# Kernel optimization log

Measured on AMD Instinct MI355X. Metric: run time of the kernel, lower is better.

The kernel has to match this reference:

```python
import jax, jax.numpy as jnp
import numpy as np

B, IN, H = 16384, 512, 512


def setup_inputs() -> dict:
    key = jax.random.key(0)
    ks = jax.random.split(key, 7)
    s_in = 1.0 / np.sqrt(IN)
    s_h = 1.0 / np.sqrt(H)
    return {
        "x": jax.random.normal(ks[0], (B, IN), jnp.float32),
        "h": jax.random.normal(ks[1], (B, H), jnp.float32),
        "c": jax.random.normal(ks[2], (B, H), jnp.float32),
        # packed gate weights, order [i, f, g, o] along last dim (4*H)
        "Wx": jax.random.normal(ks[3], (IN, 4 * H), jnp.float32) * s_in,
        "Wh": jax.random.normal(ks[4], (H, 4 * H), jnp.float32) * s_h,
        "bx": jax.random.normal(ks[5], (4 * H,), jnp.float32) * s_in,
        "bh": jax.random.normal(ks[6], (4 * H,), jnp.float32) * s_h,
    }


def reference(x, h, c, Wx, Wh, bx, bh):
    # one fused GEMM per input stream instead of 8 small linears; same math
    gates = x @ Wx + bx + h @ Wh + bh          # [B, 4H]
    gi, gf, gg, go = jnp.split(gates, 4, axis=-1)
    i = jax.nn.sigmoid(gi)
    f = jax.nn.sigmoid(gf)
    g = jnp.tanh(gg)
    o = jax.nn.sigmoid(go)
    c_new = f * c + i * g
    h_new = o * jnp.tanh(c_new)
    return (h_new, c_new)
```

## Files before the change

### kernel.cpp

```cpp
#include <hip/hip_runtime.h>
#include <hip/hip_bf16.h>

#define B_DIM   16384
#define IN_DIM  512
#define H_DIM   512
#define K_DIM   1024
#define N4H     2048
#define BH      (B_DIM * H_DIM)

typedef __attribute__((ext_vector_type(8))) short  short8;
typedef __attribute__((ext_vector_type(4))) short  short4v;
typedef __attribute__((ext_vector_type(4))) float  f32x4;

__device__ inline void async_load16(const void* g, void* l) {
    __builtin_amdgcn_global_load_lds(
        (const __attribute__((address_space(1))) void*)g,
        (__attribute__((address_space(3)))       void*)l, 16, 0, 0);
}

__device__ inline short bf16bits(float f) {
    __hip_bfloat16 b = __float2bfloat16(f);
    return *reinterpret_cast<short*>(&b);
}

__device__ inline float sigmoidf_(float v) {
    return 1.0f / (1.0f + __expf(-v));
}
__device__ inline float tanhf_(float v) {
    v = fminf(fmaxf(v, -30.f), 30.f);
    float e = __expf(2.f * v);
    return (e - 1.f) / (e + 1.f);
}

__global__ __launch_bounds__(256) void prep_all(
    const float* __restrict__ Wx, const float* __restrict__ Wh,
    const float* __restrict__ bx, const float* __restrict__ bh,
    const float* __restrict__ x,  const float* __restrict__ h,
    __hip_bfloat16* __restrict__ Wt, __hip_bfloat16* __restrict__ Axh,
    float* __restrict__ bias_p) {
    const int bid = blockIdx.x;
    const int t   = threadIdx.x;

    if (bid < 2048) {
        __shared__ __hip_bfloat16 tile[32][33];
        const int bk = bid & 31;
        const int bn = bid >> 5;
        const int kb = bk * 32, nb = bn * 32;
#pragma unroll
        for (int r = 0; r < 4; ++r) {
            int k_loc = r * 8 + (t >> 5);
            int n_loc = t & 31;
            int kg = kb + k_loc;
            float v = (kg < IN_DIM) ? Wx[(size_t)kg * N4H + nb + n_loc]
                                    : Wh[(size_t)(kg - IN_DIM) * N4H + nb + n_loc];
            tile[k_loc][n_loc] = __float2bfloat16(v);
        }
        __syncthreads();
        {
            int n_loc = t >> 3;
            int k_loc = (t & 7) * 4;
            int ng = nb + n_loc;
            int g  = ng >> 9;
            int c  = ng & 511;
            int row_out = (c >> 5) * 128 + g * 32 + (c & 31);
            short4v v4;
            v4.x = *reinterpret_cast<short*>(&tile[k_loc + 0][n_loc]);
            v4.y = *reinterpret_cast<short*>(&tile[k_loc + 1][n_loc]);
            v4.z = *reinterpret_cast<short*>(&tile[k_loc + 2][n_loc]);
            v4.w = *reinterpret_cast<short*>(&tile[k_loc + 3][n_loc]);
            *(short4v*)&Wt[(size_t)row_out * K_DIM + kb + k_loc] = v4;
        }
        if (bid < 8) {
            int ng = bid * 256 + t;
            int g  = ng >> 9;
            int c  = ng & 511;
            int ro = (c >> 5) * 128 + g * 32 + (c & 31);
            bias_p[ro] = bx[ng] + bh[ng];
        }
    } else {
        const int ab = bid - 2048;
        const int kq = t;
        const float* src = (kq < 128) ? (x + kq * 4)
                                      : (h + (size_t)(kq - 128) * 4);
#pragma unroll
        for (int j = 0; j < 8; ++j) {
            int m = ab * 8 + j;
            float4 v = *(const float4*)(src + (size_t)m * 512);
            short4v sv;
            sv.x = bf16bits(v.x);
            sv.y = bf16bits(v.y);
            sv.z = bf16bits(v.z);
            sv.w = bf16bits(v.w);
            *(short4v*)&Axh[(size_t)m * K_DIM + kq * 4] = sv;
        }
    }
}

__global__ __launch_bounds__(256, 3) void lstm_gemm(
    const float* __restrict__ c_in,
    const __hip_bfloat16* __restrict__ Axh,
    const __hip_bfloat16* __restrict__ Wt,
    const float* __restrict__ bias_p,
    float* __restrict__ out) {
    __shared__ __hip_bfloat16 lds_a[128 * 32];
    __shared__ __hip_bfloat16 lds_b[128 * 32];

    const int tid   = threadIdx.x;
    const int w     = tid >> 6;
    const int lane  = tid & 63;
    const int col16 = lane & 15;
    const int quad  = lane >> 4;

    const int jb    = blockIdx.x;
    const int xcd   = jb & 7;
    const int local = jb >> 3;
    const int bm    = xcd * 16 + (local >> 4);
    const int bn    = local & 15;

    f32x4 acc[2][8];
#pragma unroll
    for (int mi = 0; mi < 2; ++mi)
#pragma unroll
        for (int ni = 0; ni < 8; ++ni)
            acc[mi][ni] = (f32x4){0.f, 0.f, 0.f, 0.f};

    const __hip_bfloat16* Ab = Axh + (size_t)bm * 128 * K_DIM;
    const __hip_bfloat16* Bb = Wt  + (size_t)bn * 128 * K_DIM;

    const int s0 = w * 128 + lane;
    const int s1 = s0 + 64;
    const int r0 = s0 >> 2, r1 = s1 >> 2;
    const int q0 = ((s0 & 3) - ((r0 >> 1) & 3)) & 3;
    const int q1 = ((s1 & 3) - ((r1 >> 1) & 3)) & 3;
    const size_t ga0 = (size_t)r0 * K_DIM + q0 * 8;
    const size_t ga1 = (size_t)r1 * K_DIM + q1 * 8;
    __hip_bfloat16* la0 = lds_a + w * 1024;
    __hip_bfloat16* la1 = lds_a + w * 1024 + 512;
    __hip_bfloat16* lb0 = lds_b + w * 1024;
    __hip_bfloat16* lb1 = lds_b + w * 1024 + 512;

    int aoff[2], boff[8];
#pragma unroll
    for (int mi = 0; mi < 2; ++mi) {
        int r = w * 32 + mi * 16 + col16;
        aoff[mi] = (r * 4 + ((quad + ((r >> 1) & 3)) & 3)) * 16;
    }
#pragma unroll
    for (int ni = 0; ni < 8; ++ni) {
        int r = ni * 16 + col16;
        boff[ni] = (r * 4 + ((quad + ((r >> 1) & 3)) & 3)) * 16;
    }
    const char* lap = (const char*)lds_a;
    const char* lbp = (const char*)lds_b;

    for (int kt = 0; kt < 32; ++kt) {
        const int kb = kt * 32;
        async_load16(Ab + ga0 + kb, la0);
        async_load16(Ab + ga1 + kb, la1);
        async_load16(Bb + ga0 + kb, lb0);
        async_load16(Bb + ga1 + kb, lb1);
        __syncthreads();

        short8 afr[2], bfr[8];
#pragma unroll
        for (int mi = 0; mi < 2; ++mi)
            afr[mi] = *(const short8*)(lap + aoff[mi]);
#pragma unroll
        for (int ni = 0; ni < 8; ++ni)
            bfr[ni] = *(const short8*)(lbp + boff[ni]);
#pragma unroll
        for (int mi = 0; mi < 2; ++mi)
#pragma unroll
            for (int ni = 0; ni < 8; ++ni)
                acc[mi][ni] = __builtin_amdgcn_mfma_f32_16x16x32_bf16(
                    afr[mi], bfr[ni], acc[mi][ni], 0, 0, 0);
        __syncthreads();
    }

    float bias_v[4][2];
#pragma unroll
    for (int g = 0; g < 4; ++g)
#pragma unroll
        for (int h2 = 0; h2 < 2; ++h2)
            bias_v[g][h2] = bias_p[bn * 128 + g * 32 + h2 * 16 + col16];

#pragma unroll
    for (int mi = 0; mi < 2; ++mi) {
#pragma unroll
        for (int reg = 0; reg < 4; ++reg) {
            const int m_g = bm * 128 + w * 32 + mi * 16 + quad * 4 + reg;
#pragma unroll
            for (int h2 = 0; h2 < 2; ++h2) {
                const int hc_g = bn * 32 + h2 * 16 + col16;
                float gi = acc[mi][0 + h2][reg] + bias_v[0][h2];
                float gf = acc[mi][2 + h2][reg] + bias_v[1][h2];
                float gg = acc[mi][4 + h2][reg] + bias_v[2][h2];
                float go = acc[mi][6 + h2][reg] + bias_v[3][h2];
                float iv = sigmoidf_(gi);
                float fv = sigmoidf_(gf);
                float gv = tanhf_(gg);
                float ov = sigmoidf_(go);
                float co = c_in[(size_t)m_g * H_DIM + hc_g];
                float cn = fv * co + iv * gv;
                float hn = ov * tanhf_(cn);
                out[(size_t)m_g * H_DIM + hc_g]      = hn;
                out[BH + (size_t)m_g * H_DIM + hc_g] = cn;
            }
        }
    }
}

__global__ __launch_bounds__(256) void prep_weights_fb(
    const float* __restrict__ Wx, const float* __restrict__ Wh,
    const float* __restrict__ bx, const float* __restrict__ bh,
    __hip_bfloat16* __restrict__ Wt, float* __restrict__ bias_p) {
    __shared__ __hip_bfloat16 tile[32][33];
    const int bid = blockIdx.x;
    const int bk  = bid & 31;
    const int bn  = bid >> 5;
    const int t   = threadIdx.x;
    const int kb  = bk * 32, nb = bn * 32;
#pragma unroll
    for (int r = 0; r < 4; ++r) {
        int k_loc = r * 8 + (t >> 5);
        int n_loc = t & 31;
        int kg = kb + k_loc;
        float v = (kg < IN_DIM) ? Wx[(size_t)kg * N4H + nb + n_loc]
                                : Wh[(size_t)(kg - IN_DIM) * N4H + nb + n_loc];
        tile[k_loc][n_loc] = __float2bfloat16(v);
    }
    __syncthreads();
    {
        int n_loc = t >> 3;
        int k_loc = (t & 7) * 4;
        int ng = nb + n_loc;
        int g  = ng >> 9;
        int c  = ng & 511;
        int row_out = (c >> 5) * 128 + g * 32 + (c & 31);
        short4v v4;
        v4.x = *reinterpret_cast<short*>(&tile[k_loc + 0][n_loc]);
        v4.y = *reinterpret_cast<short*>(&tile[k_loc + 1][n_loc]);
        v4.z = *reinterpret_cast<short*>(&tile[k_loc + 2][n_loc]);
        v4.w = *reinterpret_cast<short*>(&tile[k_loc + 3][n_loc]);
        *(short4v*)&Wt[(size_t)row_out * K_DIM + kb + k_loc] = v4;
    }
    if (bid < 8) {
        int ng = bid * 256 + t;
        int g  = ng >> 9;
        int c  = ng & 511;
        int ro = (c >> 5) * 128 + g * 32 + (c & 31);
        bias_p[ro] = bx[ng] + bh[ng];
    }
}

__global__ __launch_bounds__(256, 3) void lstm_gemm_fb(
    const float* __restrict__ x, const float* __restrict__ h,
    const float* __restrict__ c_in,
    const __hip_bfloat16* __restrict__ Wt, const float* __restrict__ bias_p,
    float* __restrict__ out) {
    __shared__ __hip_bfloat16 lds_a[128 * 32];
    __shared__ __hip_bfloat16 lds_b[128 * 32];
    const int tid   = threadIdx.x;
    const int bn    = blockIdx.x & 15;
    const int bm    = blockIdx.x >> 4;
    const int w     = tid >> 6;
    const int lane  = tid & 63;
    const int col16 = lane & 15;
    const int quad  = lane >> 4;
    f32x4 acc[2][8];
#pragma unroll
    for (int mi = 0; mi < 2; ++mi)
#pragma unroll
        for (int ni = 0; ni < 8; ++ni)
            acc[mi][ni] = (f32x4){0.f, 0.f, 0.f, 0.f};
    const __hip_bfloat16* wt_base = Wt + (size_t)(bn * 128) * K_DIM;
    const int chunk0 = w * 2;
    const int e0     = chunk0 * 512 + lane * 8;
    const int bn_loc0 = e0 >> 5, bk_off0 = e0 & 31;
    const int e1     = (chunk0 + 1) * 512 + lane * 8;
    const int bn_loc1 = e1 >> 5, bk_off1 = e1 & 31;
    for (int kt = 0; kt < 32; ++kt) {
        const int kb = kt * 32;
        const float* aptr;
        int koff;
        if (kb < IN_DIM) { aptr = x; koff = kb; }
        else             { aptr = h; koff = kb - IN_DIM; }
        async_load16(wt_base + (size_t)bn_loc0 * K_DIM + kb + bk_off0,
                     (void*)(lds_b + chunk0 * 512));
        async_load16(wt_base + (size_t)bn_loc1 * K_DIM + kb + bk_off1,
                     (void*)(lds_b + (chunk0 + 1) * 512));
        float4 av[4];
#pragma unroll
        for (int j = 0; j < 4; ++j) {
            int cch = j * 256 + tid;
            int row = cch >> 3;
            int kq  = (cch & 7) * 4;
            av[j] = *(const float4*)(aptr + (size_t)(bm * 128 + row) * IN_DIM
                                     + koff + kq);
        }
#pragma unroll
        for (int j = 0; j < 4; ++j) {
            int cch = j * 256 + tid;
            int row = cch >> 3;
            int kq  = (cch & 7) * 4;
            short4v sv;
            sv.x = bf16bits(av[j].x);
            sv.y = bf16bits(av[j].y);
            sv.z = bf16bits(av[j].z);
            sv.w = bf16bits(av[j].w);
            *(short4v*)&lds_a[row * 32 + kq] = sv;
        }
        __syncthreads();
        short8 afr[2], bfr[8];
#pragma unroll
        for (int mi = 0; mi < 2; ++mi)
            afr[mi] = *(const short8*)&lds_a[(w * 32 + mi * 16 + col16) * 32 + quad * 8];
#pragma unroll
        for (int ni = 0; ni < 8; ++ni)
            bfr[ni] = *(const short8*)&lds_b[(ni * 16 + col16) * 32 + quad * 8];
#pragma unroll
        for (int mi = 0; mi < 2; ++mi)
#pragma unroll
            for (int ni = 0; ni < 8; ++ni)
                acc[mi][ni] = __builtin_amdgcn_mfma_f32_16x16x32_bf16(
                    afr[mi], bfr[ni], acc[mi][ni], 0, 0, 0);
        __syncthreads();
    }
    float bias_v[4][2];
#pragma unroll
    for (int g = 0; g < 4; ++g)
#pragma unroll
        for (int h2 = 0; h2 < 2; ++h2)
            bias_v[g][h2] = bias_p[bn * 128 + g * 32 + h2 * 16 + col16];
#pragma unroll
    for (int mi = 0; mi < 2; ++mi) {
#pragma unroll
        for (int reg = 0; reg < 4; ++reg) {
            const int m_g = bm * 128 + w * 32 + mi * 16 + quad * 4 + reg;
#pragma unroll
            for (int h2 = 0; h2 < 2; ++h2) {
                const int hc_g = bn * 32 + h2 * 16 + col16;
                float gi = acc[mi][0 + h2][reg] + bias_v[0][h2];
                float gf = acc[mi][2 + h2][reg] + bias_v[1][h2];
                float gg = acc[mi][4 + h2][reg] + bias_v[2][h2];
                float go = acc[mi][6 + h2][reg] + bias_v[3][h2];
                float iv = sigmoidf_(gi);
                float fv = sigmoidf_(gf);
                float gv = tanhf_(gg);
                float ov = sigmoidf_(go);
                float co = c_in[(size_t)m_g * H_DIM + hc_g];
                float cn = fv * co + iv * gv;
                float hn = ov * tanhf_(cn);
                out[(size_t)m_g * H_DIM + hc_g]      = hn;
                out[BH + (size_t)m_g * H_DIM + hc_g] = cn;
            }
        }
    }
}

extern "C" void kernel_launch(void* const* d_in, const int* in_sizes, int n_in,
                              void* d_out, int out_size, void* d_ws, size_t ws_size,
                              hipStream_t stream) {
    const float* x  = (const float*)d_in[0];
    const float* h  = (const float*)d_in[1];
    const float* c  = (const float*)d_in[2];
    const float* Wx = (const float*)d_in[3];
    const float* Wh = (const float*)d_in[4];
    const float* bx = (const float*)d_in[5];
    const float* bh = (const float*)d_in[6];

    const size_t wtBytes  = (size_t)N4H * K_DIM * 2;
    const size_t axhBytes = (size_t)B_DIM * K_DIM * 2;
    const size_t need     = wtBytes + axhBytes + (size_t)N4H * 4;

    if (ws_size >= need) {
        __hip_bfloat16* Wt  = (__hip_bfloat16*)d_ws;
        __hip_bfloat16* Axh = (__hip_bfloat16*)((char*)d_ws + wtBytes);
        float* bias_p = (float*)((char*)d_ws + wtBytes + axhBytes);
        prep_all<<<4096, 256, 0, stream>>>(Wx, Wh, bx, bh, x, h, Wt, Axh, bias_p);
        lstm_gemm<<<2048, 256, 0, stream>>>(c, Axh, Wt, bias_p, (float*)d_out);
    } else {
        __hip_bfloat16* Wt = (__hip_bfloat16*)d_ws;
        float* bias_p = (float*)((char*)d_ws + wtBytes);
        prep_weights_fb<<<2048, 256, 0, stream>>>(Wx, Wh, bx, bh, Wt, bias_p);
        lstm_gemm_fb<<<2048, 256, 0, stream>>>(x, h, c, Wt, bias_p, (float*)d_out);
    }
}
```

Baseline: 250.8 us.

## Switch LSTM GEMM to 32x32x16 MFMA with BK=64 and XOR-swizzled LDS

Replaces the 16x16x32 bf16 MFMA tiling with 32x32x16 MFMA, so each wave computes a 32x128 tile with four accumulators. The K step per iteration doubles to 64, which halves the number of barrier pairs, and the LDS layout moves to an XOR swizzle to avoid bank conflicts. The c_in values are now prefetched into registers before the main loop so their latency overlaps the GEMM. The occupancy hint rises to 4 blocks per CU, which risks register spills with 64 accumulator floats plus 16 prefetched c values per thread.

```diff
diff --git a/kernel.cpp b/kernel.cpp
--- a/kernel.cpp
+++ b/kernel.cpp
@@ -8,9 +8,10 @@
 #define N4H     2048
 #define BH      (B_DIM * H_DIM)
 
-typedef __attribute__((ext_vector_type(8))) short  short8;
-typedef __attribute__((ext_vector_type(4))) short  short4v;
-typedef __attribute__((ext_vector_type(4))) float  f32x4;
+typedef __attribute__((ext_vector_type(8)))  short  short8;
+typedef __attribute__((ext_vector_type(4)))  short  short4v;
+typedef __attribute__((ext_vector_type(4)))  float  f32x4;
+typedef __attribute__((ext_vector_type(16))) float  f32x16;
 
 __device__ inline void async_load16(const void* g, void* l) {
     __builtin_amdgcn_global_load_lds(
@@ -96,20 +97,20 @@
     }
 }
 
-__global__ __launch_bounds__(256, 3) void lstm_gemm(
+__global__ __launch_bounds__(256, 4) void lstm_gemm(
     const float* __restrict__ c_in,
     const __hip_bfloat16* __restrict__ Axh,
     const __hip_bfloat16* __restrict__ Wt,
     const float* __restrict__ bias_p,
     float* __restrict__ out) {
-    __shared__ __hip_bfloat16 lds_a[128 * 32];
-    __shared__ __hip_bfloat16 lds_b[128 * 32];
-
-    const int tid   = threadIdx.x;
-    const int w     = tid >> 6;
-    const int lane  = tid & 63;
-    const int col16 = lane & 15;
-    const int quad  = lane >> 4;
+    __shared__ __hip_bfloat16 lds_a[128 * 64];
+    __shared__ __hip_bfloat16 lds_b[128 * 64];
+
+    const int tid  = threadIdx.x;
+    const int w    = tid >> 6;
+    const int lane = tid & 63;
+    const int l31  = lane & 31;
+    const int half = lane >> 5;
 
     const int jb    = blockIdx.x;
     const int xcd   = jb & 7;
@@ -117,96 +118,89 @@
     const int bm    = xcd * 16 + (local >> 4);
     const int bn    = local & 15;
 
-    f32x4 acc[2][8];
-#pragma unroll
-    for (int mi = 0; mi < 2; ++mi)
-#pragma unroll
-        for (int ni = 0; ni < 8; ++ni)
-            acc[mi][ni] = (f32x4){0.f, 0.f, 0.f, 0.f};
+    f32x16 acc[4];
+#pragma unroll
+    for (int ni = 0; ni < 4; ++ni)
+#pragma unroll
+        for (int r = 0; r < 16; ++r)
+            acc[ni][r] = 0.f;
 
     const __hip_bfloat16* Ab = Axh + (size_t)bm * 128 * K_DIM;
     const __hip_bfloat16* Bb = Wt  + (size_t)bn * 128 * K_DIM;
 
-    const int s0 = w * 128 + lane;
-    const int s1 = s0 + 64;
-    const int r0 = s0 >> 2, r1 = s1 >> 2;
-    const int q0 = ((s0 & 3) - ((r0 >> 1) & 3)) & 3;
-    const int q1 = ((s1 & 3) - ((r1 >> 1) & 3)) & 3;
-    const size_t ga0 = (size_t)r0 * K_DIM + q0 * 8;
-    const size_t ga1 = (size_t)r1 * K_DIM + q1 * 8;
-    __hip_bfloat16* la0 = lds_a + w * 1024;
-    __hip_bfloat16* la1 = lds_a + w * 1024 + 512;
-    __hip_bfloat16* lb0 = lds_b + w * 1024;
-    __hip_bfloat16* lb1 = lds_b + w * 1024 + 512;
-
-    int aoff[2], boff[8];
-#pragma unroll
-    for (int mi = 0; mi < 2; ++mi) {
-        int r = w * 32 + mi * 16 + col16;
-        aoff[mi] = (r * 4 + ((quad + ((r >> 1) & 3)) & 3)) * 16;
-    }
-#pragma unroll
-    for (int ni = 0; ni < 8; ++ni) {
-        int r = ni * 16 + col16;
-        boff[ni] = (r * 4 + ((quad + ((r >> 1) & 3)) & 3)) * 16;
-    }
-    const char* lap = (const char*)lds_a;
+    const int r_base = w * 32 + (lane >> 3);
+    const int q8     = (((lane & 7) ^ ((lane >> 3) & 7)) * 8);
+    size_t g_off[4];
+    __hip_bfloat16* lA[4];
+    __hip_bfloat16* lB[4];
+#pragma unroll
+    for (int j = 0; j < 4; ++j) {
+        g_off[j] = (size_t)(r_base + j * 8) * K_DIM + q8;
+        lA[j] = lds_a + w * 2048 + j * 512;
+        lB[j] = lds_b + w * 2048 + j * 512;
+    }
+
+    int rd_off[4];
+#pragma unroll
+    for (int sk = 0; sk < 4; ++sk)
+        rd_off[sk] = l31 * 128 + (((sk * 2 + half) ^ (lane & 7)) * 16);
+
+    const int col = bn * 32 + l31;
+    float c_reg[16];
+#pragma unroll
+    for (int reg = 0; reg < 16; ++reg) {
+        int m_loc = (reg & 3) + 8 * (reg >> 2) + 4 * half;
+        c_reg[reg] = c_in[(size_t)(bm * 128 + w * 32 + m_loc) * H_DIM + col];
+    }
+
+    const char* lap = (const char*)lds_a + w * 4096;
     const char* lbp = (const char*)lds_b;
 
-    for (int kt = 0; kt < 32; ++kt) {
-        const int kb = kt * 32;
-        async_load16(Ab + ga0 + kb, la0);
-        async_load16(Ab + ga1 + kb, la1);
-        async_load16(Bb + ga0 + kb, lb0);
-        async_load16(Bb + ga1 + kb, lb1);
-        __syncthreads();
-
-        short8 afr[2], bfr[8];
-#pragma unroll
-        for (int mi = 0; mi < 2; ++mi)
-            afr[mi] = *(const short8*)(lap + aoff[mi]);
-#pragma unroll
-        for (int ni = 0; ni < 8; ++ni)
-            bfr[ni] = *(const short8*)(lbp + boff[ni]);
-#pragma unroll
-        for (int mi = 0; mi < 2; ++mi)
-#pragma unroll
-            for (int ni = 0; ni < 8; ++ni)
-                acc[mi][ni] = __builtin_amdgcn_mfma_f32_16x16x32_bf16(
-                    afr[mi], bfr[ni], acc[mi][ni], 0, 0, 0);
-        __syncthreads();
-    }
-
-    float bias_v[4][2];
+    for (int kt = 0; kt < 16; ++kt) {
+        const int kb = kt * 64;
+#pragma unroll
+        for (int j = 0; j < 4; ++j) {
+            async_load16(Ab + g_off[j] + kb, lA[j]);
+            async_load16(Bb + g_off[j] + kb, lB[j]);
+        }
+        __syncthreads();
+
+#pragma unroll
+        for (int sk = 0; sk < 4; ++sk) {
+            short8 af = *(const short8*)(lap + rd_off[sk]);
+            short8 bf0 = *(const short8*)(lbp + 0 * 4096 + rd_off[sk]);
+            short8 bf1 = *(const short8*)(lbp + 1 * 4096 + rd_off[sk]);
+            short8 bf2 = *(const short8*)(lbp + 2 * 4096 + rd_off[sk]);
+            short8 bf3 = *(const short8*)(lbp + 3 * 4096 + rd_off[sk]);
+            acc[0] = __builtin_amdgcn_mfma_f32_32x32x16_bf16(af, bf0, acc[0], 0, 0, 0);
+            acc[1] = __builtin_amdgcn_mfma_f32_32x32x16_bf16(af, bf1, acc[1], 0, 0, 0);
+            acc[2] = __builtin_amdgcn_mfma_f32_32x32x16_bf16(af, bf2, acc[2], 0, 0, 0);
+            acc[3] = __builtin_amdgcn_mfma_f32_32x32x16_bf16(af, bf3, acc[3], 0, 0, 0);
+        }
+        __syncthreads();
+    }
+
+    float bias_v[4];
 #pragma unroll
     for (int g = 0; g < 4; ++g)
-#pragma unroll
-        for (int h2 = 0; h2 < 2; ++h2)
-            bias_v[g][h2] = bias_p[bn * 128 + g * 32 + h2 * 16 + col16];
-
-#pragma unroll
-    for (int mi = 0; mi < 2; ++mi) {
-#pragma unroll
-        for (int reg = 0; reg < 4; ++reg) {
-            const int m_g = bm * 128 + w * 32 + mi * 16 + quad * 4 + reg;
-#pragma unroll
-            for (int h2 = 0; h2 < 2; ++h2) {
-                const int hc_g = bn * 32 + h2 * 16 + col16;
-                float gi = acc[mi][0 + h2][reg] + bias_v[0][h2];
-                float gf = acc[mi][2 + h2][reg] + bias_v[1][h2];
-                float gg = acc[mi][4 + h2][reg] + bias_v[2][h2];
-                float go = acc[mi][6 + h2][reg] + bias_v[3][h2];
-                float iv = sigmoidf_(gi);
-                float fv = sigmoidf_(gf);
-                float gv = tanhf_(gg);
-                float ov = sigmoidf_(go);
-                float co = c_in[(size_t)m_g * H_DIM + hc_g];
-                float cn = fv * co + iv * gv;
-                float hn = ov * tanhf_(cn);
-                out[(size_t)m_g * H_DIM + hc_g]      = hn;
-                out[BH + (size_t)m_g * H_DIM + hc_g] = cn;
-            }
-        }
+        bias_v[g] = bias_p[bn * 128 + g * 32 + l31];
+
+#pragma unroll
+    for (int reg = 0; reg < 16; ++reg) {
+        int m_loc = (reg & 3) + 8 * (reg >> 2) + 4 * half;
+        size_t m_g = (size_t)(bm * 128 + w * 32 + m_loc);
+        float gi = acc[0][reg] + bias_v[0];
+        float gf = acc[1][reg] + bias_v[1];
+        float gg = acc[2][reg] + bias_v[2];
+        float go = acc[3][reg] + bias_v[3];
+        float iv = sigmoidf_(gi);
+        float fv = sigmoidf_(gf);
+        float gv = tanhf_(gg);
+        float ov = sigmoidf_(go);
+        float cn = fv * c_reg[reg] + iv * gv;
+        float hn = ov * tanhf_(cn);
+        out[m_g * H_DIM + col]      = hn;
+        out[BH + m_g * H_DIM + col] = cn;
     }
 }
 
```

Result: slower. 281.6 us (+12.3%).

## Double-buffer LDS tiles to prefetch next K-slice during MFMA compute

Applied to the files above, without the earlier changes.

Doubles the shared-memory tiles for A and B. The loop now issues the async global-to-LDS loads for the next K tile right after the barrier, while MFMAs run on the current buffer. This cuts the barriers per iteration from two to one, and is meant to hide global load latency behind compute. The cost is LDS per block going from 16 KB to 32 KB. There is also a risk that the compiler inserts conservative vmcnt waits before the LDS reads, which would cancel the overlap.

```diff
diff --git a/kernel.cpp b/kernel.cpp
--- a/kernel.cpp
+++ b/kernel.cpp
@@ -102,8 +102,8 @@
     const __hip_bfloat16* __restrict__ Wt,
     const float* __restrict__ bias_p,
     float* __restrict__ out) {
-    __shared__ __hip_bfloat16 lds_a[128 * 32];
-    __shared__ __hip_bfloat16 lds_b[128 * 32];
+    __shared__ __hip_bfloat16 lds_a[2][128 * 32];
+    __shared__ __hip_bfloat16 lds_b[2][128 * 32];
 
     const int tid   = threadIdx.x;
     const int w     = tid >> 6;
@@ -134,10 +134,6 @@
     const int q1 = ((s1 & 3) - ((r1 >> 1) & 3)) & 3;
     const size_t ga0 = (size_t)r0 * K_DIM + q0 * 8;
     const size_t ga1 = (size_t)r1 * K_DIM + q1 * 8;
-    __hip_bfloat16* la0 = lds_a + w * 1024;
-    __hip_bfloat16* la1 = lds_a + w * 1024 + 512;
-    __hip_bfloat16* lb0 = lds_b + w * 1024;
-    __hip_bfloat16* lb1 = lds_b + w * 1024 + 512;
 
     int aoff[2], boff[8];
 #pragma unroll
@@ -150,16 +146,24 @@
         int r = ni * 16 + col16;
         boff[ni] = (r * 4 + ((quad + ((r >> 1) & 3)) & 3)) * 16;
     }
-    const char* lap = (const char*)lds_a;
-    const char* lbp = (const char*)lds_b;
+
+    async_load16(Ab + ga0, (void*)(&lds_a[0][w * 1024]));
+    async_load16(Ab + ga1, (void*)(&lds_a[0][w * 1024 + 512]));
+    async_load16(Bb + ga0, (void*)(&lds_b[0][w * 1024]));
+    async_load16(Bb + ga1, (void*)(&lds_b[0][w * 1024 + 512]));
 
     for (int kt = 0; kt < 32; ++kt) {
-        const int kb = kt * 32;
-        async_load16(Ab + ga0 + kb, la0);
-        async_load16(Ab + ga1 + kb, la1);
-        async_load16(Bb + ga0 + kb, lb0);
-        async_load16(Bb + ga1 + kb, lb1);
         __syncthreads();
+        const int p = kt & 1;
+        if (kt < 31) {
+            const int kb = (kt + 1) * 32;
+            async_load16(Ab + ga0 + kb, (void*)(&lds_a[1 - p][w * 1024]));
+            async_load16(Ab + ga1 + kb, (void*)(&lds_a[1 - p][w * 1024 + 512]));
+            async_load16(Bb + ga0 + kb, (void*)(&lds_b[1 - p][w * 1024]));
+            async_load16(Bb + ga1 + kb, (void*)(&lds_b[1 - p][w * 1024 + 512]));
+        }
+        const char* lap = (const char*)lds_a[p];
+        const char* lbp = (const char*)lds_b[p];
 
         short8 afr[2], bfr[8];
 #pragma unroll
@@ -174,7 +178,6 @@
             for (int ni = 0; ni < 8; ++ni)
                 acc[mi][ni] = __builtin_amdgcn_mfma_f32_16x16x32_bf16(
                     afr[mi], bfr[ni], acc[mi][ni], 0, 0, 0);
-        __syncthreads();
     }
 
     float bias_v[4][2];
```

After: 249.1 us. No clear change (-0.7%).
